# Optimization experiments

Measured on AMD Instinct MI355X. Metric: run time of the kernel, lower is better.

## Reference

```python
import jax, jax.numpy as jnp
import numpy as np

INPUT_DIM, PROJ_DIM, HIDDEN = 1, 16, 32
B, T = 2048, 2048


def setup_inputs() -> dict:
    key = jax.random.key(0)
    ks = jax.random.split(key, 9)
    s_in = 1.0 / np.sqrt(INPUT_DIM)
    s_h = 1.0 / np.sqrt(HIDDEN)
    s_p = 1.0 / np.sqrt(PROJ_DIM)
    return {
        "x_seq": jax.random.normal(ks[0], (B, T, INPUT_DIM), dtype=jnp.float32),
        # input_linear: Linear(input_dim, proj_dim)
        "Wp": jax.random.uniform(ks[1], (PROJ_DIM, INPUT_DIM), minval=-s_in, maxval=s_in),
        "bp": jax.random.uniform(ks[2], (PROJ_DIM,), minval=-s_in, maxval=s_in),
        # LSTM weights (PyTorch gate order i,f,g,o)
        "W_ih": jax.random.uniform(ks[3], (4 * HIDDEN, PROJ_DIM), minval=-s_h, maxval=s_h),
        "W_hh": jax.random.uniform(ks[4], (4 * HIDDEN, HIDDEN), minval=-s_h, maxval=s_h),
        "b_ih": jax.random.uniform(ks[5], (4 * HIDDEN,), minval=-s_h, maxval=s_h),
        "b_hh": jax.random.uniform(ks[6], (4 * HIDDEN,), minval=-s_h, maxval=s_h),
        # output_linear: Linear(hidden, input_dim)
        "Wo": jax.random.uniform(ks[7], (INPUT_DIM, HIDDEN), minval=-s_h, maxval=s_h),
        "bo": jax.random.uniform(ks[8], (INPUT_DIM,), minval=-s_h, maxval=s_h),
    }


def reference(x_seq, Wp, bp, W_ih, W_hh, b_ih, b_hh, Wo, bo):
    H = W_hh.shape[1]
    b, t, _ = x_seq.shape
    # input projection for all timesteps at once (same math as per-step Linear)
    # then pre-apply W_ih: [B,T,4H]
    xp = jnp.einsum("bti,pi->btp", x_seq, Wp) + bp
    gates_x = jnp.einsum("btp,gp->btg", xp, W_ih) + b_ih + b_hh
    gates_x = jnp.transpose(gates_x, (1, 0, 2))  # [T,B,4H]

    def step(carry, gx):
        h, c = carry
        gates = gx + h @ W_hh.T  # [B,4H]
        i, f, g, o = jnp.split(gates, 4, axis=-1)
        i = jax.nn.sigmoid(i)
        f = jax.nn.sigmoid(f)
        g = jnp.tanh(g)
        o = jax.nn.sigmoid(o)
        c = f * c + i * g
        h = o * jnp.tanh(c)
        return (h, c), h

    h0 = jnp.zeros((b, H), dtype=x_seq.dtype)
    c0 = jnp.zeros((b, H), dtype=x_seq.dtype)
    (_, _), hs = jax.lax.scan(step, (h0, c0), gates_x)  # hs: [T,B,H]
    outputs = jnp.einsum("tbh,oh->bto", hs, Wo) + bo  # [B,T,input_dim]
    return outputs
```

## Files before the change

### kernel.cpp

```cpp
#include <hip/hip_runtime.h>


#define BB 2048
#define TT 2048
#define HH 32

typedef _Float16 h2 __attribute__((ext_vector_type(2)));
typedef unsigned int uint2v __attribute__((ext_vector_type(2)));

__device__ __forceinline__ float gate_eval(float x, float m, float a, float b) {
    float e = __builtin_amdgcn_exp2f(x * m);
    float r = __builtin_amdgcn_rcpf(1.0f + e);
    return fmaf(a, r, b);
}

template <int CTRL>
__device__ __forceinline__ int dpp_i(int v) {
    return __builtin_amdgcn_update_dpp(0, v, CTRL, 0xf, 0xf, true);
}

template <int CTRL>
__device__ __forceinline__ float dpp_add(float v) {
    int s = __builtin_amdgcn_update_dpp(0, __float_as_int(v), CTRL, 0xf, 0xf, true);
    return v + __int_as_float(s);
}

#define DPP_XOR1 0xB1
#define DPP_XOR2 0x4E
#define DPP_ROR4 0x124
#define DPP_ROR8 0x128

__global__ __launch_bounds__(256) void lstm_fused_kernel(
    const float* __restrict__ x_seq,
    const float* __restrict__ Wp,
    const float* __restrict__ bp,
    const float* __restrict__ W_ih,
    const float* __restrict__ W_hh,
    const float* __restrict__ b_ih,
    const float* __restrict__ b_hh,
    const float* __restrict__ Wo,
    const float* __restrict__ bo,
    float* __restrict__ out)
{
    const int tid  = threadIdx.x;
    const int wave = tid >> 6;
    const int lane = tid & 63;
    const int brow = (lane >> 4) & 1;
    const int j    = (lane & 15) | ((lane >> 5) << 4);
    const int b    = blockIdx.x * 8 + wave * 2 + brow;

    const int rI = j, rF = HH + j, rG = 2 * HH + j, rO = 3 * HH + j;

    int iL0 = j;
    int iH0 = dpp_i<DPP_XOR1>(iL0);
    int iL1 = dpp_i<DPP_XOR2>(iL0), iH1 = dpp_i<DPP_XOR2>(iH0);
    int iL2 = dpp_i<DPP_ROR4>(iL0), iH2 = dpp_i<DPP_ROR4>(iH0);
    int iL3 = dpp_i<DPP_ROR4>(iL1), iH3 = dpp_i<DPP_ROR4>(iH1);
    int iL4 = dpp_i<DPP_ROR8>(iL0), iH4 = dpp_i<DPP_ROR8>(iH0);
    int iL5 = dpp_i<DPP_ROR8>(iL1), iH5 = dpp_i<DPP_ROR8>(iH1);
    int iL6 = dpp_i<DPP_ROR8>(iL2), iH6 = dpp_i<DPP_ROR8>(iH2);
    int iL7 = dpp_i<DPP_ROR8>(iL3), iH7 = dpp_i<DPP_ROR8>(iH3);

    int idx0L[8], idx1L[8], idx0H[8], idx1H[8];
    {
        const int tL[8] = {iL0, iL1, iL2, iL3, iL4, iL5, iL6, iL7};
        const int tH[8] = {iH0, iH1, iH2, iH3, iH4, iH5, iH6, iH7};
#pragma unroll
        for (int p = 0; p < 8; ++p) {
            uint2v r = __builtin_amdgcn_permlane32_swap((unsigned)tL[p], (unsigned)tL[p], false, false);
            idx0L[p] = (int)r[0]; idx1L[p] = (int)r[1];
            uint2v q = __builtin_amdgcn_permlane32_swap((unsigned)tH[p], (unsigned)tH[p], false, false);
            idx0H[p] = (int)q[0]; idx1H[p] = (int)q[1];
        }
    }

    h2 wI0[8], wI1[8], wF0[8], wF1[8], wG0[8], wG1[8], wO0[8], wO1[8];
    {
        const float* WI = W_hh + rI * HH;
        const float* WF = W_hh + rF * HH;
        const float* WG = W_hh + rG * HH;
        const float* WO = W_hh + rO * HH;
#pragma unroll
        for (int p = 0; p < 8; ++p) {
            wI0[p].x = (_Float16)WI[idx0L[p]]; wI0[p].y = (_Float16)WI[idx0H[p]];
            wI1[p].x = (_Float16)WI[idx1L[p]]; wI1[p].y = (_Float16)WI[idx1H[p]];
            wF0[p].x = (_Float16)WF[idx0L[p]]; wF0[p].y = (_Float16)WF[idx0H[p]];
            wF1[p].x = (_Float16)WF[idx1L[p]]; wF1[p].y = (_Float16)WF[idx1H[p]];
            wG0[p].x = (_Float16)WG[idx0L[p]]; wG0[p].y = (_Float16)WG[idx0H[p]];
            wG1[p].x = (_Float16)WG[idx1L[p]]; wG1[p].y = (_Float16)WG[idx1H[p]];
            wO0[p].x = (_Float16)WO[idx0L[p]]; wO0[p].y = (_Float16)WO[idx0H[p]];
            wO1[p].x = (_Float16)WO[idx1L[p]]; wO1[p].y = (_Float16)WO[idx1H[p]];
        }
    }

    float aI = 0.f, cI = 0.f, aF = 0.f, cF = 0.f;
    float aG = 0.f, cG = 0.f, aO = 0.f, cO = 0.f;
#pragma unroll
    for (int p = 0; p < 16; ++p) {
        float wpv = Wp[p], bpv = bp[p];
        float wi = W_ih[rI * 16 + p], wf = W_ih[rF * 16 + p];
        float wg = W_ih[rG * 16 + p], wo_ = W_ih[rO * 16 + p];
        aI = fmaf(wi, wpv, aI);  cI = fmaf(wi, bpv, cI);
        aF = fmaf(wf, wpv, aF);  cF = fmaf(wf, bpv, cF);
        aG = fmaf(wg, wpv, aG);  cG = fmaf(wg, bpv, cG);
        aO = fmaf(wo_, wpv, aO); cO = fmaf(wo_, bpv, cO);
    }
    cI += b_ih[rI] + b_hh[rI];
    cF += b_ih[rF] + b_hh[rF];
    cG += b_ih[rG] + b_hh[rG];
    cO += b_ih[rO] + b_hh[rO];

    const float LOG2E = 1.44269504088896340736f;
    const float woj = Wo[j];
    const float bo0 = bo[0];

    unsigned m0[8], m1[8];
#pragma unroll
    for (int p = 0; p < 8; ++p) { m0[p] = 0u; m1[p] = 0u; }

    float c = 0.0f;
    const float* xp = x_seq + (size_t)b * TT;
    float* op = out + (size_t)b * TT;

    float4 x4 = *(const float4*)(xp);

    for (int t = 0; t < TT; t += 4) {
        const int tn = (t + 4 < TT) ? (t + 4) : t;
        float4 x4n = *(const float4*)(xp + tn);
        float outv[4];
#pragma unroll
        for (int u = 0; u < 4; ++u) {
            float xv = (u == 0) ? x4.x : (u == 1) ? x4.y : (u == 2) ? x4.z : x4.w;

            float sI0 = cI, sI1 = xv * aI;
            float sF0 = cF, sF1 = xv * aF;
            float sG0 = cG, sG1 = xv * aG;
            float sO0 = cO, sO1 = xv * aO;
#pragma unroll
            for (int p = 0; p < 8; ++p) {
                h2 h0 = __builtin_bit_cast(h2, m0[p]);
                h2 h1 = __builtin_bit_cast(h2, m1[p]);
                sI0 = __builtin_amdgcn_fdot2(wI0[p], h0, sI0, false);
                sF0 = __builtin_amdgcn_fdot2(wF0[p], h0, sF0, false);
                sG0 = __builtin_amdgcn_fdot2(wG0[p], h0, sG0, false);
                sO0 = __builtin_amdgcn_fdot2(wO0[p], h0, sO0, false);
                sI1 = __builtin_amdgcn_fdot2(wI1[p], h1, sI1, false);
                sF1 = __builtin_amdgcn_fdot2(wF1[p], h1, sF1, false);
                sG1 = __builtin_amdgcn_fdot2(wG1[p], h1, sG1, false);
                sO1 = __builtin_amdgcn_fdot2(wO1[p], h1, sO1, false);
            }

            float iv = gate_eval(sI0 + sI1, -LOG2E, 1.0f, 0.0f);
            float fv = gate_eval(sF0 + sF1, -LOG2E, 1.0f, 0.0f);
            float gv = gate_eval(sG0 + sG1, -2.0f * LOG2E, 2.0f, -1.0f);
            float ov = gate_eval(sO0 + sO1, -LOG2E, 1.0f, 0.0f);

            c = fmaf(fv, c, iv * gv);
            float th = gate_eval(c, -2.0f * LOG2E, 2.0f, -1.0f);
            float h = ov * th;

            unsigned own = (unsigned)__builtin_bit_cast(unsigned short, (_Float16)h);
            int nb = dpp_i<DPP_XOR1>((int)own);
            unsigned q0 = own | ((unsigned)nb << 16);
            unsigned q1 = (unsigned)dpp_i<DPP_XOR2>((int)q0);
            unsigned q2 = (unsigned)dpp_i<DPP_ROR4>((int)q0);
            unsigned q3 = (unsigned)dpp_i<DPP_ROR4>((int)q1);
            unsigned q4 = (unsigned)dpp_i<DPP_ROR8>((int)q0);
            unsigned q5 = (unsigned)dpp_i<DPP_ROR8>((int)q1);
            unsigned q6 = (unsigned)dpp_i<DPP_ROR8>((int)q2);
            unsigned q7 = (unsigned)dpp_i<DPP_ROR8>((int)q3);
            {
                uint2v r;
                r = __builtin_amdgcn_permlane32_swap(q0, q0, false, false); m0[0] = r[0]; m1[0] = r[1];
                r = __builtin_amdgcn_permlane32_swap(q1, q1, false, false); m0[1] = r[0]; m1[1] = r[1];
                r = __builtin_amdgcn_permlane32_swap(q2, q2, false, false); m0[2] = r[0]; m1[2] = r[1];
                r = __builtin_amdgcn_permlane32_swap(q3, q3, false, false); m0[3] = r[0]; m1[3] = r[1];
                r = __builtin_amdgcn_permlane32_swap(q4, q4, false, false); m0[4] = r[0]; m1[4] = r[1];
                r = __builtin_amdgcn_permlane32_swap(q5, q5, false, false); m0[5] = r[0]; m1[5] = r[1];
                r = __builtin_amdgcn_permlane32_swap(q6, q6, false, false); m0[6] = r[0]; m1[6] = r[1];
                r = __builtin_amdgcn_permlane32_swap(q7, q7, false, false); m0[7] = r[0]; m1[7] = r[1];
            }

            float po = woj * h;
            po = dpp_add<0x111>(po);
            po = dpp_add<0x112>(po);
            po = dpp_add<0x114>(po);
            po = dpp_add<0x118>(po);
            uint2v rr = __builtin_amdgcn_permlane32_swap(
                __float_as_uint(po), __float_as_uint(po), false, false);
            outv[u] = __uint_as_float(rr[0]) + __uint_as_float(rr[1]) + bo0;
        }
        if (lane < 32 && (lane & 15) == 15) {
            *(float4*)(op + t) = make_float4(outv[0], outv[1], outv[2], outv[3]);
        }
        x4 = x4n;
    }
}

extern "C" void kernel_launch(void* const* d_in, const int* in_sizes, int n_in,
                              void* d_out, int out_size, void* d_ws, size_t ws_size,
                              hipStream_t stream) {
    const float* x_seq = (const float*)d_in[0];
    const float* Wp    = (const float*)d_in[1];
    const float* bp    = (const float*)d_in[2];
    const float* W_ih  = (const float*)d_in[3];
    const float* W_hh  = (const float*)d_in[4];
    const float* b_ih  = (const float*)d_in[5];
    const float* b_hh  = (const float*)d_in[6];
    const float* Wo    = (const float*)d_in[7];
    const float* bo    = (const float*)d_in[8];
    float* out = (float*)d_out;

    dim3 grid(BB / 8);
    dim3 block(256);
    lstm_fused_kernel<<<grid, block, 0, stream>>>(
        x_seq, Wp, bp, W_ih, W_hh, b_ih, b_hh, Wo, bo, out);
}
```

Measured before the change: 734.0 us.

## Split LSTM K-reduction across wave halves, one batch row per wave

Each wave now handles one batch row instead of two. The 32 hidden inputs are split so each half-wave does half the recurrent dot products, with partial gate sums combined via permlane32_swap. The h broadcast uses permlane16_swap with a select, and the output reduction uses a row-broadcast DPP instead of a cross-half swap. This shortens the per-step dependency chain (8 instead of 16 fdot2 per accumulator) at the cost of twice as many waves and extra cross-lane exchanges per step.

```diff
diff --git a/kernel.cpp b/kernel.cpp
--- a/kernel.cpp
+++ b/kernel.cpp
@@ -29,6 +29,16 @@
 #define DPP_XOR2 0x4E
 #define DPP_ROR4 0x124
 #define DPP_ROR8 0x128
+
+__device__ __forceinline__ void rowswap16(unsigned q, unsigned &r0, unsigned &r1) {
+#if __has_builtin(__builtin_amdgcn_permlane16_swap)
+    uint2v r = __builtin_amdgcn_permlane16_swap(q, q, false, false);
+    r0 = r[0]; r1 = r[1];
+#else
+    r0 = q;
+    r1 = (unsigned)__builtin_amdgcn_ds_swizzle((int)q, 0x401F);
+#endif
+}
 
 __global__ __launch_bounds__(256) void lstm_fused_kernel(
     const float* __restrict__ x_seq,
@@ -45,9 +55,9 @@
     const int tid  = threadIdx.x;
     const int wave = tid >> 6;
     const int lane = tid & 63;
-    const int brow = (lane >> 4) & 1;
-    const int j    = (lane & 15) | ((lane >> 5) << 4);
-    const int b    = blockIdx.x * 8 + wave * 2 + brow;
+    const int j    = lane & 31;
+    const unsigned khalf = (unsigned)(lane >> 5);
+    const int b    = blockIdx.x * 4 + wave;
 
     const int rI = j, rF = HH + j, rG = 2 * HH + j, rO = 3 * HH + j;
 
@@ -61,20 +71,26 @@
     int iL6 = dpp_i<DPP_ROR8>(iL2), iH6 = dpp_i<DPP_ROR8>(iH2);
     int iL7 = dpp_i<DPP_ROR8>(iL3), iH7 = dpp_i<DPP_ROR8>(iH3);
 
-    int idx0L[8], idx1L[8], idx0H[8], idx1H[8];
+    int selL[8], selH[8];
+    unsigned use0;
     {
         const int tL[8] = {iL0, iL1, iL2, iL3, iL4, iL5, iL6, iL7};
         const int tH[8] = {iH0, iH1, iH2, iH3, iH4, iH5, iH6, iH7};
+        unsigned eL[8], oL[8], eH[8], oH[8];
 #pragma unroll
         for (int p = 0; p < 8; ++p) {
-            uint2v r = __builtin_amdgcn_permlane32_swap((unsigned)tL[p], (unsigned)tL[p], false, false);
-            idx0L[p] = (int)r[0]; idx1L[p] = (int)r[1];
-            uint2v q = __builtin_amdgcn_permlane32_swap((unsigned)tH[p], (unsigned)tH[p], false, false);
-            idx0H[p] = (int)q[0]; idx1H[p] = (int)q[1];
-        }
-    }
-
-    h2 wI0[8], wI1[8], wF0[8], wF1[8], wG0[8], wG1[8], wO0[8], wO1[8];
+            rowswap16((unsigned)tL[p], eL[p], oL[p]);
+            rowswap16((unsigned)tH[p], eH[p], oH[p]);
+        }
+        use0 = (((eL[0] >> 4) & 1u) == khalf) ? 1u : 0u;
+#pragma unroll
+        for (int p = 0; p < 8; ++p) {
+            selL[p] = use0 ? (int)eL[p] : (int)oL[p];
+            selH[p] = use0 ? (int)eH[p] : (int)oH[p];
+        }
+    }
+
+    h2 wI[8], wF[8], wG[8], wO[8];
     {
         const float* WI = W_hh + rI * HH;
         const float* WF = W_hh + rF * HH;
@@ -82,14 +98,10 @@
         const float* WO = W_hh + rO * HH;
 #pragma unroll
         for (int p = 0; p < 8; ++p) {
-            wI0[p].x = (_Float16)WI[idx0L[p]]; wI0[p].y = (_Float16)WI[idx0H[p]];
-            wI1[p].x = (_Float16)WI[idx1L[p]]; wI1[p].y = (_Float16)WI[idx1H[p]];
-            wF0[p].x = (_Float16)WF[idx0L[p]]; wF0[p].y = (_Float16)WF[idx0H[p]];
-            wF1[p].x = (_Float16)WF[idx1L[p]]; wF1[p].y = (_Float16)WF[idx1H[p]];
-            wG0[p].x = (_Float16)WG[idx0L[p]]; wG0[p].y = (_Float16)WG[idx0H[p]];
-            wG1[p].x = (_Float16)WG[idx1L[p]]; wG1[p].y = (_Float16)WG[idx1H[p]];
-            wO0[p].x = (_Float16)WO[idx0L[p]]; wO0[p].y = (_Float16)WO[idx0H[p]];
-            wO1[p].x = (_Float16)WO[idx1L[p]]; wO1[p].y = (_Float16)WO[idx1H[p]];
+            wI[p].x = (_Float16)WI[selL[p]]; wI[p].y = (_Float16)WI[selH[p]];
+            wF[p].x = (_Float16)WF[selL[p]]; wF[p].y = (_Float16)WF[selH[p]];
+            wG[p].x = (_Float16)WG[selL[p]]; wG[p].y = (_Float16)WG[selH[p]];
+            wO[p].x = (_Float16)WO[selL[p]]; wO[p].y = (_Float16)WO[selH[p]];
         }
     }
 
@@ -109,14 +121,18 @@
     cF += b_ih[rF] + b_hh[rF];
     cG += b_ih[rG] + b_hh[rG];
     cO += b_ih[rO] + b_hh[rO];
+    if (khalf) {
+        aI = 0.f; cI = 0.f; aF = 0.f; cF = 0.f;
+        aG = 0.f; cG = 0.f; aO = 0.f; cO = 0.f;
+    }
 
     const float LOG2E = 1.44269504088896340736f;
     const float woj = Wo[j];
     const float bo0 = bo[0];
 
-    unsigned m0[8], m1[8];
-#pragma unroll
-    for (int p = 0; p < 8; ++p) { m0[p] = 0u; m1[p] = 0u; }
+    unsigned m[8];
+#pragma unroll
+    for (int p = 0; p < 8; ++p) m[p] = 0u;
 
     float c = 0.0f;
     const float* xp = x_seq + (size_t)b * TT;
@@ -137,23 +153,37 @@
             float sG0 = cG, sG1 = xv * aG;
             float sO0 = cO, sO1 = xv * aO;
 #pragma unroll
-            for (int p = 0; p < 8; ++p) {
-                h2 h0 = __builtin_bit_cast(h2, m0[p]);
-                h2 h1 = __builtin_bit_cast(h2, m1[p]);
-                sI0 = __builtin_amdgcn_fdot2(wI0[p], h0, sI0, false);
-                sF0 = __builtin_amdgcn_fdot2(wF0[p], h0, sF0, false);
-                sG0 = __builtin_amdgcn_fdot2(wG0[p], h0, sG0, false);
-                sO0 = __builtin_amdgcn_fdot2(wO0[p], h0, sO0, false);
-                sI1 = __builtin_amdgcn_fdot2(wI1[p], h1, sI1, false);
-                sF1 = __builtin_amdgcn_fdot2(wF1[p], h1, sF1, false);
-                sG1 = __builtin_amdgcn_fdot2(wG1[p], h1, sG1, false);
-                sO1 = __builtin_amdgcn_fdot2(wO1[p], h1, sO1, false);
+            for (int p = 0; p < 8; p += 2) {
+                h2 h0 = __builtin_bit_cast(h2, m[p]);
+                h2 h1 = __builtin_bit_cast(h2, m[p + 1]);
+                sI0 = __builtin_amdgcn_fdot2(wI[p],     h0, sI0, false);
+                sF0 = __builtin_amdgcn_fdot2(wF[p],     h0, sF0, false);
+                sG0 = __builtin_amdgcn_fdot2(wG[p],     h0, sG0, false);
+                sO0 = __builtin_amdgcn_fdot2(wO[p],     h0, sO0, false);
+                sI1 = __builtin_amdgcn_fdot2(wI[p + 1], h1, sI1, false);
+                sF1 = __builtin_amdgcn_fdot2(wF[p + 1], h1, sF1, false);
+                sG1 = __builtin_amdgcn_fdot2(wG[p + 1], h1, sG1, false);
+                sO1 = __builtin_amdgcn_fdot2(wO[p + 1], h1, sO1, false);
             }
 
-            float iv = gate_eval(sI0 + sI1, -LOG2E, 1.0f, 0.0f);
-            float fv = gate_eval(sF0 + sF1, -LOG2E, 1.0f, 0.0f);
-            float gv = gate_eval(sG0 + sG1, -2.0f * LOG2E, 2.0f, -1.0f);
-            float ov = gate_eval(sO0 + sO1, -LOG2E, 1.0f, 0.0f);
+            float pI = sI0 + sI1, pF = sF0 + sF1, pG = sG0 + sG1, pO = sO0 + sO1;
+            uint2v mI = __builtin_amdgcn_permlane32_swap(
+                __float_as_uint(pI), __float_as_uint(pI), false, false);
+            uint2v mF = __builtin_amdgcn_permlane32_swap(
+                __float_as_uint(pF), __float_as_uint(pF), false, false);
+            uint2v mG = __builtin_amdgcn_permlane32_swap(
+                __float_as_uint(pG), __float_as_uint(pG), false, false);
+            uint2v mO = __builtin_amdgcn_permlane32_swap(
+                __float_as_uint(pO), __float_as_uint(pO), false, false);
+            float gI = __uint_as_float(mI[0]) + __uint_as_float(mI[1]);
+            float gF = __uint_as_float(mF[0]) + __uint_as_float(mF[1]);
+            float gG = __uint_as_float(mG[0]) + __uint_as_float(mG[1]);
+            float gO = __uint_as_float(mO[0]) + __uint_as_float(mO[1]);
+
+            float iv = gate_eval(gI, -LOG2E, 1.0f, 0.0f);
+            float fv = gate_eval(gF, -LOG2E, 1.0f, 0.0f);
+            float gv = gate_eval(gG, -2.0f * LOG2E, 2.0f, -1.0f);
+            float ov = gate_eval(gO, -LOG2E, 1.0f, 0.0f);
 
             c = fmaf(fv, c, iv * gv);
             float th = gate_eval(c, -2.0f * LOG2E, 2.0f, -1.0f);
@@ -170,15 +200,15 @@
             unsigned q6 = (unsigned)dpp_i<DPP_ROR8>((int)q2);
             unsigned q7 = (unsigned)dpp_i<DPP_ROR8>((int)q3);
             {
-                uint2v r;
-                r = __builtin_amdgcn_permlane32_swap(q0, q0, false, false); m0[0] = r[0]; m1[0] = r[1];
-                r = __builtin_amdgcn_permlane32_swap(q1, q1, false, false); m0[1] = r[0]; m1[1] = r[1];
-                r = __builtin_amdgcn_permlane32_swap(q2, q2, false, false); m0[2] = r[0]; m1[2] = r[1];
-                r = __builtin_amdgcn_permlane32_swap(q3, q3, false, false); m0[3] = r[0]; m1[3] = r[1];
-                r = __builtin_amdgcn_permlane32_swap(q4, q4, false, false); m0[4] = r[0]; m1[4] = r[1];
-                r = __builtin_amdgcn_permlane32_swap(q5, q5, false, false); m0[5] = r[0]; m1[5] = r[1];
-                r = __builtin_amdgcn_permlane32_swap(q6, q6, false, false); m0[6] = r[0]; m1[6] = r[1];
-                r = __builtin_amdgcn_permlane32_swap(q7, q7, false, false); m0[7] = r[0]; m1[7] = r[1];
+                unsigned r0, r1;
+                rowswap16(q0, r0, r1); m[0] = use0 ? r0 : r1;
+                rowswap16(q1, r0, r1); m[1] = use0 ? r0 : r1;
+                rowswap16(q2, r0, r1); m[2] = use0 ? r0 : r1;
+                rowswap16(q3, r0, r1); m[3] = use0 ? r0 : r1;
+                rowswap16(q4, r0, r1); m[4] = use0 ? r0 : r1;
+                rowswap16(q5, r0, r1); m[5] = use0 ? r0 : r1;
+                rowswap16(q6, r0, r1); m[6] = use0 ? r0 : r1;
+                rowswap16(q7, r0, r1); m[7] = use0 ? r0 : r1;
             }
 
             float po = woj * h;
@@ -186,11 +216,10 @@
             po = dpp_add<0x112>(po);
             po = dpp_add<0x114>(po);
             po = dpp_add<0x118>(po);
-            uint2v rr = __builtin_amdgcn_permlane32_swap(
-                __float_as_uint(po), __float_as_uint(po), false, false);
-            outv[u] = __uint_as_float(rr[0]) + __uint_as_float(rr[1]) + bo0;
-        }
-        if (lane < 32 && (lane & 15) == 15) {
+            po = dpp_add<0x142>(po);
+            outv[u] = po + bo0;
+        }
+        if (lane == 31) {
             *(float4*)(op + t) = make_float4(outv[0], outv[1], outv[2], outv[3]);
         }
         x4 = x4n;
@@ -211,7 +240,7 @@
     const float* bo    = (const float*)d_in[8];
     float* out = (float*)d_out;
 
-    dim3 grid(BB / 8);
+    dim3 grid(BB / 4);
     dim3 block(256);
     lstm_fused_kernel<<<grid, block, 0, stream>>>(
         x_seq, Wp, bp, W_ih, W_hh, b_ih, b_hh, Wo, bo, out);
```

Result: slower. 1.217 ms (+65.8%).
